# Performance work log

Measured on AMD Instinct MI355X. Metric: run time of the kernel, lower is better.

## Reference

```python
import jax, jax.numpy as jnp
import numpy as np

D_MODEL = 1024
FF = 4096
E = 8
TOP_K = 2
CAP_FACTOR = 1.25
B, T = 4, 2048


def setup_inputs() -> dict:
    key = jax.random.key(0)
    ks = jax.random.split(key, 7)
    s = 0.02
    return {
        "x": jax.random.normal(ks[0], (B, T, D_MODEL), jnp.float32),
        "gate_w": jax.random.normal(ks[1], (D_MODEL, E), jnp.float32) * s,
        "gate_b": jnp.zeros((E,), jnp.float32),
        "w1": jax.random.normal(ks[2], (E, D_MODEL, FF), jnp.float32) * s,
        "b1": jnp.zeros((E, FF), jnp.float32),
        "w2": jax.random.normal(ks[3], (E, FF, D_MODEL), jnp.float32) * s,
        "b2": jnp.zeros((E, D_MODEL), jnp.float32),
    }


def _moe_forward(x, gate_w, gate_b, w1, b1, w2, b2):
    Bb, Tt, d = x.shape
    S = Bb * Tt
    C = int(CAP_FACTOR * S / E)  # static expert capacity (1280)
    xf = x.reshape(S, d)

    # Router: softmax then top-k, renormalized
    logits = xf @ gate_w + gate_b                      # [S, E]
    probs = jax.nn.softmax(logits, axis=1)
    topk_p, topk_i = jax.lax.top_k(probs, TOP_K)       # [S, K]
    topk_pn = topk_p / jnp.sum(topk_p, axis=1, keepdims=True)

    rows = jnp.arange(S)
    # per-(token, expert) combine weight; top_k gives distinct experts per token
    w_te = jnp.zeros((S, E), xf.dtype).at[rows[:, None], topk_i].set(topk_pn)
    mask = jnp.zeros((S, E), bool).at[rows[:, None], topk_i].set(True)

    # capacity drop: keep first C selected tokens per expert (token-index order)
    rank = jnp.cumsum(mask.astype(jnp.int32), axis=0)  # [S, E], 1-based
    slot = jnp.where(mask & (rank <= C), rank - 1, C)  # dump slot = C
    e_grid = jnp.broadcast_to(jnp.arange(E), (S, E))
    t_grid = jnp.broadcast_to(rows[:, None], (S, E))
    buf = jnp.full((E, C + 1), S, jnp.int32).at[e_grid, slot].set(t_grid)
    idx = buf[:, :C]                                   # [E, C], pad id = S
    valid = idx < S

    # gather -> grouped expert MLP -> weight -> scatter-add
    x_pad = jnp.concatenate([xf, jnp.zeros((1, d), xf.dtype)], axis=0)
    xin = x_pad[idx]                                   # [E, C, d]
    h = jax.nn.relu(jnp.einsum('ecd,edh->ech', xin, w1) + b1[:, None, :])
    out = jnp.einsum('ech,ehd->ecd', h, w2) + b2[:, None, :]

    w_pad = jnp.concatenate([w_te, jnp.zeros((1, E), xf.dtype)], axis=0)
    tok_w = w_pad[idx, jnp.arange(E)[:, None]]         # [E, C]
    out = out * jnp.where(valid, tok_w, 0.0)[:, :, None]

    final = jnp.zeros((S + 1, d), xf.dtype).at[idx.reshape(-1)].add(out.reshape(-1, d))[:S]
    return final.reshape(Bb, Tt, d)


def reference(x, gate_w, gate_b, w1, b1, w2, b2):
    return _moe_forward(x, gate_w, gate_b, w1, b1, w2, b2)
```

## Files before the change

kernel.cpp:

```cpp
#include <hip/hip_runtime.h>
#include <hip/hip_bf16.h>
#include <stdint.h>

#define S_TOK 8192
#define DM    1024
#define FFD   4096
#define NE    8
#define CAP   1280

typedef __attribute__((ext_vector_type(8))) __bf16 bf16x8;
typedef __attribute__((ext_vector_type(8))) unsigned short u16x8;
typedef __attribute__((ext_vector_type(4))) float f32x4;

__device__ __forceinline__ unsigned short f2bf(float f) {
    unsigned u = __float_as_uint(f);
    unsigned r = (u + 0x7FFFu + ((u >> 16) & 1u)) >> 16;
    return (unsigned short)r;
}

__device__ __forceinline__ void gload_lds16(const void* g, void* l) {
    __builtin_amdgcn_global_load_lds(
        (const __attribute__((address_space(1))) void*)g,
        (__attribute__((address_space(3))) void*)l, 16, 0, 0);
}

__global__ __launch_bounds__(256) void gate_kernel(
    const float* __restrict__ x, const float* __restrict__ gw,
    const float* __restrict__ gb, int2* __restrict__ tops, float2* __restrict__ wts)
{
    int wave = threadIdx.x >> 6, lane = threadIdx.x & 63;
    int t = blockIdx.x * 4 + wave;
    float acc[NE] = {0,0,0,0,0,0,0,0};
    const float* xr = x + (size_t)t * DM;
    for (int it = 0; it < DM / 64; ++it) {
        int d = it * 64 + lane;
        float xv = xr[d];
        const float4* g4 = (const float4*)(gw + (size_t)d * NE);
        float4 a = g4[0], b = g4[1];
        acc[0] += xv * a.x; acc[1] += xv * a.y; acc[2] += xv * a.z; acc[3] += xv * a.w;
        acc[4] += xv * b.x; acc[5] += xv * b.y; acc[6] += xv * b.z; acc[7] += xv * b.w;
    }
#pragma unroll
    for (int e = 0; e < NE; ++e)
#pragma unroll
        for (int off = 32; off > 0; off >>= 1)
            acc[e] += __shfl_down(acc[e], off, 64);
    if (lane == 0) {
        float lg[NE];
#pragma unroll
        for (int e = 0; e < NE; ++e) lg[e] = acc[e] + gb[e];
        int e1 = 0; float m1 = lg[0];
#pragma unroll
        for (int e = 1; e < NE; ++e) if (lg[e] > m1) { m1 = lg[e]; e1 = e; }
        int e2 = -1; float m2 = -1e30f;
#pragma unroll
        for (int e = 0; e < NE; ++e) if (e != e1 && lg[e] > m2) { m2 = lg[e]; e2 = e; }
        float p1 = 1.f / (1.f + expf(m2 - m1));
        tops[t] = make_int2(e1, e2);
        wts[t] = make_float2(p1, 1.f - p1);
    }
}

__global__ __launch_bounds__(512) void route_scan(
    const int2* __restrict__ tops, const float2* __restrict__ wts,
    int* __restrict__ idxl, float* __restrict__ tokw)
{
    int e = threadIdx.x >> 6, lane = threadIdx.x & 63;
    for (int s = lane; s < CAP; s += 64) { idxl[e * CAP + s] = S_TOK; tokw[e * CAP + s] = 0.f; }
    int base = 0;
    for (int ch = 0; ch < S_TOK / 64; ++ch) {
        int t = ch * 64 + lane;
        int2 te = tops[t];
        float2 wv = wts[t];
        bool m1 = (te.x == e), m2 = (te.y == e);
        bool a = m1 || m2;
        unsigned long long bal = __ballot(a);
        int pre = __popcll(bal & ((1ull << lane) - 1ull));
        if (a) {
            int slot = base + pre;
            if (slot < CAP) { idxl[e * CAP + slot] = t; tokw[e * CAP + slot] = m1 ? wv.x : wv.y; }
        }
        base += __popcll(bal);
    }
}

__global__ __launch_bounds__(256) void cvt_x_kernel(const float* __restrict__ x,
                                                    unsigned short* __restrict__ xp)
{
    if (blockIdx.x == (S_TOK * DM / 8) / 256) {
        if (threadIdx.x < DM / 8) {
            u16x8 z = {0,0,0,0,0,0,0,0};
            *(u16x8*)(xp + (size_t)S_TOK * DM + threadIdx.x * 8) = z;
        }
        return;
    }
    size_t i = (size_t)blockIdx.x * 256 + threadIdx.x;
    const float4* s = (const float4*)(x + i * 8);
    float4 a = s[0], b = s[1];
    u16x8 o;
    o[0]=f2bf(a.x); o[1]=f2bf(a.y); o[2]=f2bf(a.z); o[3]=f2bf(a.w);
    o[4]=f2bf(b.x); o[5]=f2bf(b.y); o[6]=f2bf(b.z); o[7]=f2bf(b.w);
    *(u16x8*)(xp + i * 8) = o;
}

__global__ __launch_bounds__(256) void transpose_cvt(
    const float* __restrict__ src, unsigned short* __restrict__ dst, int K, int N)
{
    __shared__ float tile[64][65];
    size_t ebase = (size_t)blockIdx.z * K * N;
    int k0 = blockIdx.y * 64, n0 = blockIdx.x * 64;
    int t = threadIdx.x;
    int tr = t >> 4, tc = (t & 15) * 4;
#pragma unroll
    for (int rr = 0; rr < 4; ++rr) {
        int k = tr + rr * 16;
        float4 v = *(const float4*)(src + ebase + (size_t)(k0 + k) * N + n0 + tc);
        tile[tc + 0][k] = v.x; tile[tc + 1][k] = v.y; tile[tc + 2][k] = v.z; tile[tc + 3][k] = v.w;
    }
    __syncthreads();
    int nr = t >> 3, kc = (t & 7) * 8;
#pragma unroll
    for (int ww = 0; ww < 2; ++ww) {
        int n = nr + ww * 32;
        u16x8 o;
#pragma unroll
        for (int q = 0; q < 8; ++q) o[q] = f2bf(tile[n][kc + q]);
        *(u16x8*)(dst + ebase + (size_t)(n0 + n) * K + k0 + kc) = o;
    }
}

__global__ __launch_bounds__(256) void moe_gemm1(
    const unsigned short* __restrict__ xpad, const unsigned short* __restrict__ w1t,
    const float* __restrict__ b1, const int* __restrict__ idxl, unsigned short* __restrict__ h)
{
    __shared__ unsigned short As[128 * 64];
    __shared__ unsigned short Bs[128 * 64];
    const int MT = CAP / 128, NT = FFD / 128;
    const int NWG = NE * MT * NT;
    int wgid = (blockIdx.x & 7) * (NWG / 8) + (blockIdx.x >> 3);
    int e = wgid / (MT * NT); int r = wgid % (MT * NT);
    int tm = r / NT, tn = r % NT;
    int t = threadIdx.x, wave = t >> 6, lane = t & 63;

    const unsigned short* asrc[4]; const unsigned short* bsrc[4];
#pragma unroll
    for (int i = 0; i < 4; ++i) {
        int row = (i * 256 + t) >> 3;
        int g = idxl[e * CAP + tm * 128 + row];
        asrc[i] = xpad + (size_t)g * DM + (t & 7) * 8;
        bsrc[i] = w1t + ((size_t)e * FFD + tn * 128 + row) * DM + (t & 7) * 8;
    }
    f32x4 acc[4][4] = {};
    int wr = wave >> 1, wc = wave & 1;
    int a_off = (wr * 64 + (lane & 15)) * 64 + (lane >> 4) * 8;
    int b_off = (wc * 64 + (lane & 15)) * 64 + (lane >> 4) * 8;

    for (int kt = 0; kt < DM / 64; ++kt) {
#pragma unroll
        for (int i = 0; i < 4; ++i) {
            gload_lds16(asrc[i] + kt * 64, As + (i * 4 + wave) * 512);
            gload_lds16(bsrc[i] + kt * 64, Bs + (i * 4 + wave) * 512);
        }
        __syncthreads();
#pragma unroll
        for (int kk = 0; kk < 2; ++kk) {
            bf16x8 af[4], bfr[4];
#pragma unroll
            for (int m = 0; m < 4; ++m) af[m]  = *(const bf16x8*)(As + a_off + m * 1024 + kk * 32);
#pragma unroll
            for (int n = 0; n < 4; ++n) bfr[n] = *(const bf16x8*)(Bs + b_off + n * 1024 + kk * 32);
#pragma unroll
            for (int m = 0; m < 4; ++m)
#pragma unroll
                for (int n = 0; n < 4; ++n)
                    acc[m][n] = __builtin_amdgcn_mfma_f32_16x16x32_bf16(af[m], bfr[n], acc[m][n], 0, 0, 0);
        }
        __syncthreads();
    }
    int col0 = tn * 128 + wc * 64 + (lane & 15);
    int row0 = tm * 128 + wr * 64 + ((lane >> 4) * 4);
    float bv[4];
#pragma unroll
    for (int n = 0; n < 4; ++n) bv[n] = b1[(size_t)e * FFD + col0 + n * 16];
#pragma unroll
    for (int m = 0; m < 4; ++m)
#pragma unroll
        for (int j = 0; j < 4; ++j) {
            int row = row0 + m * 16 + j;
            size_t hb = ((size_t)e * CAP + row) * FFD;
#pragma unroll
            for (int n = 0; n < 4; ++n) {
                float v = acc[m][n][j] + bv[n];
                v = fmaxf(v, 0.f);
                h[hb + col0 + n * 16] = f2bf(v);
            }
        }
}

#define KSPLIT 2
#define KHALF  (FFD / KSPLIT)
__global__ __launch_bounds__(256) void moe_gemm2(
    const unsigned short* __restrict__ h, const unsigned short* __restrict__ w2t,
    const float* __restrict__ b2, const int* __restrict__ idxl, const float* __restrict__ tokw,
    float* __restrict__ out)
{
    __shared__ unsigned short As[128 * 64];
    __shared__ unsigned short Bs[128 * 64];
    const int MT = CAP / 128, NT = DM / 128;
    const int NWG = NE * KSPLIT * MT * NT;
    int wgid = (blockIdx.x & 7) * (NWG / 8) + (blockIdx.x >> 3);
    int e = wgid / (KSPLIT * MT * NT); int r = wgid % (KSPLIT * MT * NT);
    int kz = r / (MT * NT); int r2 = r % (MT * NT);
    int tm = r2 / NT, tn = r2 % NT;
    int t = threadIdx.x, wave = t >> 6, lane = t & 63;

    const unsigned short* asrc[4]; const unsigned short* bsrc[4];
#pragma unroll
    for (int i = 0; i < 4; ++i) {
        int row = (i * 256 + t) >> 3;
        asrc[i] = h   + ((size_t)e * CAP + tm * 128 + row) * FFD + kz * KHALF + (t & 7) * 8;
        bsrc[i] = w2t + ((size_t)e * DM  + tn * 128 + row) * FFD + kz * KHALF + (t & 7) * 8;
    }
    f32x4 acc[4][4] = {};
    int wr = wave >> 1, wc = wave & 1;
    int a_off = (wr * 64 + (lane & 15)) * 64 + (lane >> 4) * 8;
    int b_off = (wc * 64 + (lane & 15)) * 64 + (lane >> 4) * 8;

    for (int kt = 0; kt < KHALF / 64; ++kt) {
#pragma unroll
        for (int i = 0; i < 4; ++i) {
            gload_lds16(asrc[i] + kt * 64, As + (i * 4 + wave) * 512);
            gload_lds16(bsrc[i] + kt * 64, Bs + (i * 4 + wave) * 512);
        }
        __syncthreads();
#pragma unroll
        for (int kk = 0; kk < 2; ++kk) {
            bf16x8 af[4], bfr[4];
#pragma unroll
            for (int m = 0; m < 4; ++m) af[m]  = *(const bf16x8*)(As + a_off + m * 1024 + kk * 32);
#pragma unroll
            for (int n = 0; n < 4; ++n) bfr[n] = *(const bf16x8*)(Bs + b_off + n * 1024 + kk * 32);
#pragma unroll
            for (int m = 0; m < 4; ++m)
#pragma unroll
                for (int n = 0; n < 4; ++n)
                    acc[m][n] = __builtin_amdgcn_mfma_f32_16x16x32_bf16(af[m], bfr[n], acc[m][n], 0, 0, 0);
        }
        __syncthreads();
    }
    int col0 = tn * 128 + wc * 64 + (lane & 15);
    int row0 = tm * 128 + wr * 64 + ((lane >> 4) * 4);
    float bv[4];
#pragma unroll
    for (int n = 0; n < 4; ++n) bv[n] = (kz == 0) ? b2[(size_t)e * DM + col0 + n * 16] : 0.f;
#pragma unroll
    for (int m = 0; m < 4; ++m)
#pragma unroll
        for (int j = 0; j < 4; ++j) {
            int row = row0 + m * 16 + j;
            int tok = idxl[e * CAP + row];
            float w = tokw[e * CAP + row];
            if (w != 0.f) {
                float* orow = out + (size_t)tok * DM;
#pragma unroll
                for (int n = 0; n < 4; ++n)
                    atomicAdd(orow + col0 + n * 16, (acc[m][n][j] + bv[n]) * w);
            }
        }
}

extern "C" void kernel_launch(void* const* d_in, const int* in_sizes, int n_in,
                              void* d_out, int out_size, void* d_ws, size_t ws_size,
                              hipStream_t stream) {
    (void)in_sizes; (void)n_in; (void)ws_size;
    const float* x  = (const float*)d_in[0];
    const float* gw = (const float*)d_in[1];
    const float* gb = (const float*)d_in[2];
    const float* w1 = (const float*)d_in[3];
    const float* b1 = (const float*)d_in[4];
    const float* w2 = (const float*)d_in[5];
    const float* b2 = (const float*)d_in[6];
    float* out = (float*)d_out;

    char* ws = (char*)d_ws;
    unsigned short* w1t  = (unsigned short*)(ws);
    unsigned short* w2t  = (unsigned short*)(ws + 67108864);
    unsigned short* xpad = (unsigned short*)(ws + 134217728);
    unsigned short* hbuf = (unsigned short*)(ws + 150996992);
    int2*   tops = (int2*)  (ws + 234883072);
    float2* wtsp = (float2*)(ws + 234948608);
    int*    idxl = (int*)   (ws + 235014144);
    float*  tokw = (float*) (ws + 235055104);

    hipMemsetAsync(d_out, 0, (size_t)out_size * sizeof(float), stream);

    gate_kernel<<<S_TOK / 4, 256, 0, stream>>>(x, gw, gb, tops, wtsp);
    route_scan<<<1, 512, 0, stream>>>(tops, wtsp, idxl, tokw);
    cvt_x_kernel<<<(S_TOK * DM / 8) / 256 + 1, 256, 0, stream>>>(x, xpad);
    transpose_cvt<<<dim3(FFD / 64, DM / 64, NE), 256, 0, stream>>>(w1, w1t, DM, FFD);
    transpose_cvt<<<dim3(DM / 64, FFD / 64, NE), 256, 0, stream>>>(w2, w2t, FFD, DM);

    moe_gemm1<<<NE * (CAP / 128) * (FFD / 128), 256, 0, stream>>>(xpad, w1t, b1, idxl, hbuf);
    moe_gemm2<<<NE * KSPLIT * (CAP / 128) * (DM / 128), 256, 0, stream>>>(hbuf, w2t, b2, idxl, tokw, out);
}
```

Measured before the change: 750.4 us.

## Parallelize routing scan across blocks and remap GEMM tile order for locality

The single-block serial routing scan over all 8192 tokens is replaced by three kernels: a per-chunk histogram, a small prefix-offset kernel, and a parallel scatter over 16 blocks. This is meant to remove a long serial single-workgroup stage from the critical path, at the cost of two extra kernel launches. Separately, the GEMM1 and GEMM2 workgroup-to-tile mappings are reordered into small M×N groups so that concurrently running workgroups share A and B tiles in cache.

```diff
diff --git a/kernel.cpp b/kernel.cpp
--- a/kernel.cpp
+++ b/kernel.cpp
@@ -7,6 +7,7 @@
 #define FFD   4096
 #define NE    8
 #define CAP   1280
+#define NCH   16
 
 typedef __attribute__((ext_vector_type(8))) __bf16 bf16x8;
 typedef __attribute__((ext_vector_type(8))) unsigned short u16x8;
@@ -61,19 +62,49 @@
     }
 }
 
-__global__ __launch_bounds__(512) void route_scan(
+__global__ __launch_bounds__(512) void route_hist(
+    const int2* __restrict__ tops, int* __restrict__ cnt,
+    int* __restrict__ idxl, float* __restrict__ tokw)
+{
+    int e = threadIdx.x >> 6, lane = threadIdx.x & 63;
+    int c = blockIdx.x;
+    for (int i = blockIdx.x * 512 + threadIdx.x; i < NE * CAP; i += NCH * 512) {
+        idxl[i] = S_TOK; tokw[i] = 0.f;
+    }
+    int n = 0;
+#pragma unroll
+    for (int sub = 0; sub < 8; ++sub) {
+        int t = c * 512 + sub * 64 + lane;
+        int2 te = tops[t];
+        bool a = (te.x == e) || (te.y == e);
+        n += __popcll(__ballot(a));
+    }
+    if (lane == 0) cnt[c * NE + e] = n;
+}
+
+__global__ void route_offset(const int* __restrict__ cnt, int* __restrict__ baseArr)
+{
+    int e = threadIdx.x;
+    if (e < NE) {
+        int run = 0;
+        for (int c = 0; c < NCH; ++c) { baseArr[c * NE + e] = run; run += cnt[c * NE + e]; }
+    }
+}
+
+__global__ __launch_bounds__(512) void route_scatter(
     const int2* __restrict__ tops, const float2* __restrict__ wts,
-    int* __restrict__ idxl, float* __restrict__ tokw)
+    const int* __restrict__ baseArr, int* __restrict__ idxl, float* __restrict__ tokw)
 {
     int e = threadIdx.x >> 6, lane = threadIdx.x & 63;
-    for (int s = lane; s < CAP; s += 64) { idxl[e * CAP + s] = S_TOK; tokw[e * CAP + s] = 0.f; }
-    int base = 0;
-    for (int ch = 0; ch < S_TOK / 64; ++ch) {
-        int t = ch * 64 + lane;
+    int c = blockIdx.x;
+    int base = baseArr[c * NE + e];
+#pragma unroll
+    for (int sub = 0; sub < 8; ++sub) {
+        int t = c * 512 + sub * 64 + lane;
         int2 te = tops[t];
         float2 wv = wts[t];
-        bool m1 = (te.x == e), m2 = (te.y == e);
-        bool a = m1 || m2;
+        bool m1 = (te.x == e);
+        bool a = m1 || (te.y == e);
         unsigned long long bal = __ballot(a);
         int pre = __popcll(bal & ((1ull << lane) - 1ull));
         if (a) {
@@ -139,7 +170,8 @@
     const int NWG = NE * MT * NT;
     int wgid = (blockIdx.x & 7) * (NWG / 8) + (blockIdx.x >> 3);
     int e = wgid / (MT * NT); int r = wgid % (MT * NT);
-    int tm = r / NT, tn = r % NT;
+    int tnc = r / (MT * 4); int q = r % (MT * 4);
+    int tm = q >> 2, tn = tnc * 4 + (q & 3);
     int t = threadIdx.x, wave = t >> 6, lane = t & 63;
 
     const unsigned short* asrc[4]; const unsigned short* bsrc[4];
@@ -211,7 +243,9 @@
     int wgid = (blockIdx.x & 7) * (NWG / 8) + (blockIdx.x >> 3);
     int e = wgid / (KSPLIT * MT * NT); int r = wgid % (KSPLIT * MT * NT);
     int kz = r / (MT * NT); int r2 = r % (MT * NT);
-    int tm = r2 / NT, tn = r2 % NT;
+    int p = r2 / 20; int q = r2 % 20;
+    int tm = (p >> 1) * 5 + (q >> 2);
+    int tn = (p & 1) * 4 + (q & 3);
     int t = threadIdx.x, wave = t >> 6, lane = t & 63;
 
     const unsigned short* asrc[4]; const unsigned short* bsrc[4];
@@ -291,11 +325,15 @@
     float2* wtsp = (float2*)(ws + 234948608);
     int*    idxl = (int*)   (ws + 235014144);
     float*  tokw = (float*) (ws + 235055104);
+    int*    cnt  = (int*)   (ws + 235096064);
+    int*    bas  = (int*)   (ws + 235096576);
 
     hipMemsetAsync(d_out, 0, (size_t)out_size * sizeof(float), stream);
 
     gate_kernel<<<S_TOK / 4, 256, 0, stream>>>(x, gw, gb, tops, wtsp);
-    route_scan<<<1, 512, 0, stream>>>(tops, wtsp, idxl, tokw);
+    route_hist<<<NCH, 512, 0, stream>>>(tops, cnt, idxl, tokw);
+    route_offset<<<1, 64, 0, stream>>>(cnt, bas);
+    route_scatter<<<NCH, 512, 0, stream>>>(tops, wtsp, bas, idxl, tokw);
     cvt_x_kernel<<<(S_TOK * DM / 8) / 256 + 1, 256, 0, stream>>>(x, xpad);
     transpose_cvt<<<dim3(FFD / 64, DM / 64, NE), 256, 0, stream>>>(w1, w1t, DM, FFD);
     transpose_cvt<<<dim3(DM / 64, FFD / 64, NE), 256, 0, stream>>>(w2, w2t, FFD, DM);
```

New measurement: 696.1 us. 1.08x faster.
